# Kernel tuning notes

Measured on AMD Instinct MI355X. Metric: run time of the kernel, lower is better.

Reference implementation:

```python
import jax, jax.numpy as jnp
import numpy as np

ROUTE_SCALE = 2.5
TOP_K = 2
N_EXPERTS = 16


def setup_inputs() -> dict:
    key = jax.random.key(0)
    ks = jax.random.split(key, 8)
    B, T, D, I, E = 2, 1024, 768, 384, N_EXPERTS
    s = 0.02
    return {
        "x": jax.random.normal(ks[0], (B, T, D), dtype=jnp.float32),
        "gate_w": jax.random.normal(ks[1], (E, D), dtype=jnp.float32) * s,
        "sg_w": jax.random.normal(ks[2], (I, D), dtype=jnp.float32) * s,
        "su_w": jax.random.normal(ks[3], (I, D), dtype=jnp.float32) * s,
        "sd_w": jax.random.normal(ks[4], (D, I), dtype=jnp.float32) * s,
        "rg_w": jax.random.normal(ks[5], (E, I, D), dtype=jnp.float32) * s,
        "ru_w": jax.random.normal(ks[6], (E, I, D), dtype=jnp.float32) * s,
        "rd_w": jax.random.normal(ks[7], (E, D, I), dtype=jnp.float32) * s,
    }


def _moe_forward(x, gate_w, sg_w, su_w, sd_w, rg_w, ru_w, rd_w):
    B, T, D = x.shape
    flat = x.reshape(-1, D)  # (N, D), N = B*T

    # ---- shared expert (SwiGLU FFN) ----
    g = flat @ sg_w.T
    u = flat @ su_w.T
    shared_out = (jax.nn.silu(g) * u) @ sd_w.T  # (N, D)

    # ---- gate: softmax(fp32) -> top-k -> renormalize ----
    logits = (flat @ gate_w.T) * ROUTE_SCALE  # (N, E)
    scores = jax.nn.softmax(logits.astype(jnp.float32), axis=-1)
    topk_w, topk_i = jax.lax.top_k(scores, TOP_K)  # (N, K)
    topk_w = topk_w / jnp.sum(topk_w, axis=-1, keepdims=True)
    topk_w = topk_w.astype(x.dtype)

    # aux load-balancing loss
    one_hot = jax.nn.one_hot(topk_i, N_EXPERTS, dtype=jnp.float32)  # (N, K, E)
    mask = one_hot.sum(axis=1)  # (N, E)
    f = mask.mean(axis=0)
    p = scores.mean(axis=0)
    aux_loss = jnp.sum(f * p) * N_EXPERTS

    # combine weights per (token, expert): sum_k w_k * [idx_k == e]
    combine = jnp.einsum("nk,nke->ne", topk_w, one_hot.astype(x.dtype))  # (N, E)

    # ---- routed experts as batched (grouped) SwiGLU GEMMs ----
    rg = jnp.einsum("nd,eid->nei", flat, rg_w)  # (N, E, I)
    ru = jnp.einsum("nd,eid->nei", flat, ru_w)
    rh = jax.nn.silu(rg) * ru  # (N, E, I)
    eo = jnp.einsum("nei,edi->ned", rh, rd_w)  # (N, E, D)
    routed_out = jnp.einsum("ned,ne->nd", eo, combine)  # (N, D)

    out = (shared_out + routed_out).reshape(B, T, D)
    return out, aux_loss


def reference(x, gate_w, sg_w, su_w, sd_w, rg_w, ru_w, rd_w):
    return _moe_forward(x, gate_w, sg_w, su_w, sd_w, rg_w, ru_w, rd_w)
```

## Files before the change

### kernel.cpp

```cpp
#include <hip/hip_runtime.h>
#include <math.h>

#define NTOK 2048
#define DDIM 768
#define IDIM 384
#define NEXP 16
#define XS_LD 776
#define HS_LD 392
#define NRT_MAX 144
#define NSHT 64
#define NWORK ((NSHT + NRT_MAX) * 6)
#define CHUNK (NWORK / 8)

typedef __attribute__((ext_vector_type(8))) short short8;
typedef __attribute__((ext_vector_type(4))) float f32x4;

__device__ __forceinline__ unsigned short f2bf(float f) {
    unsigned int u = __float_as_uint(f);
    unsigned int r = (u + 0x7fffu + ((u >> 16) & 1u)) >> 16;
    return (unsigned short)r;
}

#define WS_XB   1048576u
#define WS_W1F  4194304u
#define WS_WDF  24248320u
#define WS_H    34275328u

__global__ __launch_bounds__(256) void zero_init_kernel(
    float4* __restrict__ out4, int n4,
    int* counts, int* cursor, int* offs, float* p_sum) {
    int i = blockIdx.x * 256 + threadIdx.x;
    if (i < n4) out4[i] = make_float4(0.f, 0.f, 0.f, 0.f);
    if (blockIdx.x == 0) {
        int t = threadIdx.x;
        if (t < 16) { counts[t] = 0; cursor[t] = 0; p_sum[t] = 0.f; }
        if (t < 17) offs[t] = 0;
    }
}

__global__ __launch_bounds__(256) void conv_all_kernel(
    const float* __restrict__ x,
    const float* __restrict__ rgw, const float* __restrict__ ruw,
    const float* __restrict__ sgw, const float* __restrict__ suw,
    const float* __restrict__ rdw, const float* __restrict__ sdw,
    unsigned short* __restrict__ xb, unsigned short* __restrict__ w1f,
    unsigned short* __restrict__ wdf) {
    int b = blockIdx.x, tid = threadIdx.x;
    const float* s;
    unsigned short* dst;
    if (b < 768) {
        int i = b * 256 + tid;
        s = x + (size_t)i * 8;
        dst = xb + (size_t)i * 8;
    } else if (b < 768 + 288 * 17) {
        int bb = b - 768;
        int E = bb / 288, bx = bb % 288;
        const float* gsrc = (E == 16) ? sgw : rgw + (size_t)E * (IDIM * DDIM);
        const float* usrc = (E == 16) ? suw : ruw + (size_t)E * (IDIM * DDIM);
        int i = bx * 256 + tid;
        int lane = i & 63;
        int fi = i >> 6;
        int ks = fi % 24, rg = fi / 24;
        int b16 = rg >> 1, gu = rg & 1;
        s = (gu ? usrc : gsrc)
          + (size_t)(b16 * 16 + (lane & 15)) * DDIM + ks * 32 + (lane >> 4) * 8;
        dst = w1f + (size_t)E * (DDIM * DDIM) + (size_t)i * 8;
    } else {
        int bb = b - (768 + 288 * 17);
        int E = bb / 144, bx = bb % 144;
        const float* src = (E == 16) ? sdw : rdw + (size_t)E * (DDIM * IDIM);
        int i = bx * 256 + tid;
        int lane = i & 63;
        int fi = i >> 6;
        int ks = fi % 12, cg = fi / 12;
        s = src + (size_t)(cg * 16 + (lane & 15)) * IDIM + ks * 32 + (lane >> 4) * 8;
        dst = wdf + (size_t)E * (DDIM * IDIM) + (size_t)i * 8;
    }
    float4 v0 = *(const float4*)s, v1 = *(const float4*)(s + 4);
    short8 o;
    o[0]=f2bf(v0.x); o[1]=f2bf(v0.y); o[2]=f2bf(v0.z); o[3]=f2bf(v0.w);
    o[4]=f2bf(v1.x); o[5]=f2bf(v1.y); o[6]=f2bf(v1.z); o[7]=f2bf(v1.w);
    *(short8*)dst = o;
}

__global__ __launch_bounds__(256) void gate_kernel(
    const float* __restrict__ x, const float* __restrict__ gate_w,
    int* __restrict__ topk_i, float* __restrict__ topk_w,
    int* __restrict__ counts, float* __restrict__ p_sum) {
    __shared__ float p_blk[16];
    __shared__ int   c_blk[16];
    int tid = threadIdx.x;
    if (tid < 16) { p_blk[tid] = 0.f; c_blk[tid] = 0; }
    __syncthreads();

    int wave = tid >> 6, lane = tid & 63;
    int n = blockIdx.x * 4 + wave;
    int e = lane >> 2, q = lane & 3;
    const float4* xr = (const float4*)(x + (size_t)n * DDIM);
    const float4* wr = (const float4*)(gate_w + (size_t)e * DDIM);
    float s = 0.f;
    #pragma unroll 4
    for (int k = q * 48; k < q * 48 + 48; ++k) {
        float4 a = xr[k], b = wr[k];
        s += a.x * b.x + a.y * b.y + a.z * b.z + a.w * b.w;
    }
    s += __shfl_xor(s, 1);
    s += __shfl_xor(s, 2);
    float logit = s * 2.5f;

    float l[16];
    #pragma unroll
    for (int j = 0; j < 16; ++j) l[j] = __shfl(logit, j * 4);

    float m = l[0];
    #pragma unroll
    for (int j = 1; j < 16; ++j) m = fmaxf(m, l[j]);
    float sum = 0.f, sc[16];
    #pragma unroll
    for (int j = 0; j < 16; ++j) { sc[j] = __expf(l[j] - m); sum += sc[j]; }
    float inv = 1.f / sum;
    #pragma unroll
    for (int j = 0; j < 16; ++j) sc[j] *= inv;

    float b0 = -1.f; int i0 = 0;
    #pragma unroll
    for (int j = 0; j < 16; ++j) if (sc[j] > b0) { b0 = sc[j]; i0 = j; }
    float b1 = -1.f; int i1 = 0;
    #pragma unroll
    for (int j = 0; j < 16; ++j) if (j != i0 && sc[j] > b1) { b1 = sc[j]; i1 = j; }
    float rs = 1.f / (b0 + b1);

    if (lane == 0) {
        topk_i[n * 2] = i0; topk_i[n * 2 + 1] = i1;
        topk_w[n * 2] = b0 * rs; topk_w[n * 2 + 1] = b1 * rs;
        atomicAdd(&c_blk[i0], 1); atomicAdd(&c_blk[i1], 1);
        #pragma unroll
        for (int j = 0; j < 16; ++j) atomicAdd(&p_blk[j], sc[j]);
    }
    __syncthreads();
    if (tid < 16) {
        atomicAdd(&p_sum[tid], p_blk[tid]);
        atomicAdd(&counts[tid], c_blk[tid]);
    }
}

__global__ __launch_bounds__(256) void route_kernel(
    const int* __restrict__ counts, const float* __restrict__ p_sum,
    const int* __restrict__ topk_i, const float* __restrict__ topk_w,
    int* __restrict__ offs, int* __restrict__ perm_t, float* __restrict__ perm_w,
    int* __restrict__ tile_e, int* __restrict__ tile_m, int* __restrict__ n_rt,
    float* __restrict__ out_aux) {
    __shared__ int s_off[17];
    __shared__ int s_cur[16];
    int tid = threadIdx.x;
    if (tid < 16) s_cur[tid] = 0;
    if (tid == 0) {
        int acc = 0, n = 0;
        float a = 0.f;
        for (int e = 0; e < 16; ++e) {
            int c = counts[e];
            s_off[e] = acc; offs[e] = acc;
            a += (float)c * p_sum[e];
            for (int t = 0; t < c; t += 32) { tile_e[n] = e; tile_m[n] = acc + t; ++n; }
            acc += c;
        }
        s_off[16] = acc; offs[16] = acc;
        *n_rt = n;
        out_aux[0] = a * 16.f / ((float)NTOK * (float)NTOK);
    }
    __syncthreads();
    for (int n0 = tid; n0 < NTOK; n0 += 256) {
        #pragma unroll
        for (int k = 0; k < 2; ++k) {
            int e = topk_i[n0 * 2 + k];
            int pos = atomicAdd(&s_cur[e], 1);
            int s = s_off[e] + pos;
            perm_t[s] = n0;
            perm_w[s] = topk_w[n0 * 2 + k];
        }
    }
}

__device__ __forceinline__ void swz_decode(int lid, int& bx, int& y) {
    int wid = (lid & 7) * CHUNK + (lid >> 3);
    bx = wid / 6;
    y = wid - bx * 6;
}

__global__ __launch_bounds__(256, 3) void p1_kernel(
    const unsigned short* __restrict__ xb, const unsigned short* __restrict__ w1f,
    const int* __restrict__ perm_t,
    const int* __restrict__ offs, const int* __restrict__ counts,
    const int* __restrict__ tile_e, const int* __restrict__ tile_m,
    const int* __restrict__ n_rt,
    unsigned short* __restrict__ h) {
    __shared__ unsigned short xs[32 * XS_LD];
    __shared__ int s_tok[32];
    __shared__ int s_hrow[32];

    int tid = threadIdx.x;
    int bx, y;
    swz_decode(blockIdx.x, bx, y);
    int e;
    if (bx < NSHT) {
        e = 16;
        if (tid < 32) { int t = bx * 32 + tid; s_tok[tid] = t; s_hrow[tid] = 4096 + t; }
    } else {
        int r = bx - NSHT;
        if (r >= *n_rt) return;
        e = tile_e[r];
        int m0 = tile_m[r];
        int end = offs[e] + counts[e];
        if (tid < 32) {
            int slot = m0 + tid;
            bool v = slot < end;
            s_tok[tid]  = v ? perm_t[slot] : 0;
            s_hrow[tid] = v ? slot : 6144 + tid;
        }
    }
    __syncthreads();

    for (int c = tid; c < 32 * 96; c += 256) {
        int row = c / 96, off = (c - row * 96) * 8;
        *(short8*)(xs + row * XS_LD + off) =
            *(const short8*)(xb + (size_t)s_tok[row] * DDIM + off);
    }
    __syncthreads();

    int lane = tid & 63, wave = tid >> 6;
    int lr = lane & 15, kg = (lane >> 4) * 8, jrow = (lane >> 4) * 4;

    const unsigned short* pg = w1f + ((((size_t)e * 48 + (y * 8 + wave * 2    )) * 24) * 64 + lane) * 8;
    const unsigned short* pu = w1f + ((((size_t)e * 48 + (y * 8 + wave * 2 + 1)) * 24) * 64 + lane) * 8;

    f32x4 accg0 = (f32x4)0.f, accg1 = (f32x4)0.f, accu0 = (f32x4)0.f, accu1 = (f32x4)0.f;
    for (int ks = 0; ks < 24; ++ks) {
        short8 a0 = *(const short8*)(xs + lr * XS_LD + ks * 32 + kg);
        short8 a1 = *(const short8*)(xs + (16 + lr) * XS_LD + ks * 32 + kg);
        short8 bg = *(const short8*)(pg + (size_t)ks * 512);
        short8 bu = *(const short8*)(pu + (size_t)ks * 512);
        accg0 = __builtin_amdgcn_mfma_f32_16x16x32_bf16(a0, bg, accg0, 0, 0, 0);
        accg1 = __builtin_amdgcn_mfma_f32_16x16x32_bf16(a1, bg, accg1, 0, 0, 0);
        accu0 = __builtin_amdgcn_mfma_f32_16x16x32_bf16(a0, bu, accu0, 0, 0, 0);
        accu1 = __builtin_amdgcn_mfma_f32_16x16x32_bf16(a1, bu, accu1, 0, 0, 0);
    }

    int colg = y * 64 + wave * 16 + lr;
    #pragma unroll
    for (int m = 0; m < 2; ++m) {
        #pragma unroll
        for (int j = 0; j < 4; ++j) {
            int tl = m * 16 + jrow + j;
            float g = m ? accg1[j] : accg0[j];
            float u = m ? accu1[j] : accu0[j];
            float hv = g / (1.f + __expf(-g)) * u;
            h[(size_t)s_hrow[tl] * IDIM + colg] = f2bf(hv);
        }
    }
}

__global__ __launch_bounds__(256, 4) void p2_kernel(
    const unsigned short* __restrict__ h, const unsigned short* __restrict__ wdf,
    const int* __restrict__ perm_t, const float* __restrict__ perm_w,
    const int* __restrict__ offs, const int* __restrict__ counts,
    const int* __restrict__ tile_e, const int* __restrict__ tile_m,
    const int* __restrict__ n_rt,
    float* __restrict__ out) {
    __shared__ unsigned short hs[32 * HS_LD];
    __shared__ int   s_tok[32];
    __shared__ float s_w[32];
    __shared__ int   s_arow[32];

    int tid = threadIdx.x;
    int bx, y;
    swz_decode(blockIdx.x, bx, y);
    int e;
    if (bx < NSHT) {
        e = 16;
        if (tid < 32) {
            int t = bx * 32 + tid;
            s_tok[tid] = t; s_w[tid] = 1.f; s_arow[tid] = 4096 + t;
        }
    } else {
        int r = bx - NSHT;
        if (r >= *n_rt) return;
        e = tile_e[r];
        int m0 = tile_m[r];
        int end = offs[e] + counts[e];
        if (tid < 32) {
            int slot = m0 + tid;
            bool v = slot < end;
            s_tok[tid]  = v ? perm_t[slot] : 0;
            s_w[tid]    = v ? perm_w[slot] : 0.f;
            s_arow[tid] = v ? slot : offs[e];
        }
    }
    __syncthreads();

    for (int c = tid; c < 32 * 48; c += 256) {
        int row = c / 48, off = (c - row * 48) * 8;
        *(short8*)(hs + row * HS_LD + off) =
            *(const short8*)(h + (size_t)s_arow[row] * IDIM + off);
    }
    __syncthreads();

    int lane = tid & 63, wave = tid >> 6;
    int lr = lane & 15, kg = (lane >> 4) * 8, jrow = (lane >> 4) * 4;

    const unsigned short* p0 = wdf + ((((size_t)e * 48 + (y * 8 + wave * 2    )) * 12) * 64 + lane) * 8;
    const unsigned short* p1 = wdf + ((((size_t)e * 48 + (y * 8 + wave * 2 + 1)) * 12) * 64 + lane) * 8;

    f32x4 acc00 = (f32x4)0.f, acc01 = (f32x4)0.f, acc10 = (f32x4)0.f, acc11 = (f32x4)0.f;
    for (int ks = 0; ks < 12; ++ks) {
        short8 a0 = *(const short8*)(hs + lr * HS_LD + ks * 32 + kg);
        short8 a1 = *(const short8*)(hs + (16 + lr) * HS_LD + ks * 32 + kg);
        short8 b0 = *(const short8*)(p0 + (size_t)ks * 512);
        short8 b1 = *(const short8*)(p1 + (size_t)ks * 512);
        acc00 = __builtin_amdgcn_mfma_f32_16x16x32_bf16(a0, b0, acc00, 0, 0, 0);
        acc01 = __builtin_amdgcn_mfma_f32_16x16x32_bf16(a1, b0, acc01, 0, 0, 0);
        acc10 = __builtin_amdgcn_mfma_f32_16x16x32_bf16(a0, b1, acc10, 0, 0, 0);
        acc11 = __builtin_amdgcn_mfma_f32_16x16x32_bf16(a1, b1, acc11, 0, 0, 0);
    }

    int col0 = y * 128 + wave * 32 + lr;
    #pragma unroll
    for (int m = 0; m < 2; ++m) {
        #pragma unroll
        for (int j = 0; j < 4; ++j) {
            int tl = m * 16 + jrow + j;
            float w = s_w[tl];
            if (w == 0.f) continue;
            float* orow = out + (size_t)s_tok[tl] * DDIM;
            float v0 = m ? acc01[j] : acc00[j];
            float v1 = m ? acc11[j] : acc10[j];
            atomicAdd(orow + col0,      w * v0);
            atomicAdd(orow + col0 + 16, w * v1);
        }
    }
}

extern "C" void kernel_launch(void* const* d_in, const int* in_sizes, int n_in,
                              void* d_out, int out_size, void* d_ws, size_t ws_size,
                              hipStream_t stream) {
    const float* x      = (const float*)d_in[0];
    const float* gate_w = (const float*)d_in[1];
    const float* sg_w   = (const float*)d_in[2];
    const float* su_w   = (const float*)d_in[3];
    const float* sd_w   = (const float*)d_in[4];
    const float* rg_w   = (const float*)d_in[5];
    const float* ru_w   = (const float*)d_in[6];
    const float* rd_w   = (const float*)d_in[7];
    float* out = (float*)d_out;

    char* ws = (char*)d_ws;
    int*   counts = (int*)(ws + 0);
    int*   cursor = (int*)(ws + 64);
    int*   offs   = (int*)(ws + 128);
    float* p_sum  = (float*)(ws + 256);
    int*   n_rt   = (int*)(ws + 320);
    int*   topk_i = (int*)(ws + 512);
    float* topk_w = (float*)(ws + 16896);
    int*   perm_t = (int*)(ws + 33280);
    float* perm_w = (float*)(ws + 49664);
    int*   tile_e = (int*)(ws + 66048);
    int*   tile_m = (int*)(ws + 66688);
    unsigned short* xb  = (unsigned short*)(ws + WS_XB);
    unsigned short* w1f = (unsigned short*)(ws + WS_W1F);
    unsigned short* wdf = (unsigned short*)(ws + WS_WDF);
    unsigned short* hbuf= (unsigned short*)(ws + WS_H);

    zero_init_kernel<<<1536, 256, 0, stream>>>(
        (float4*)out, NTOK * DDIM / 4, counts, cursor, offs, p_sum);

    conv_all_kernel<<<768 + 288 * 17 + 144 * 17, 256, 0, stream>>>(
        x, rg_w, ru_w, sg_w, su_w, rd_w, sd_w, xb, w1f, wdf);

    gate_kernel<<<NTOK / 4, 256, 0, stream>>>(x, gate_w, topk_i, topk_w, counts, p_sum);

    route_kernel<<<1, 256, 0, stream>>>(counts, p_sum, topk_i, topk_w,
                                        offs, perm_t, perm_w, tile_e, tile_m, n_rt,
                                        out + (size_t)NTOK * DDIM);

    p1_kernel<<<NWORK, 256, 0, stream>>>(
        xb, w1f, perm_t, offs, counts, tile_e, tile_m, n_rt, hbuf);
    p2_kernel<<<NWORK, 256, 0, stream>>>(
        hbuf, wdf, perm_t, perm_w, offs, counts, tile_e, tile_m, n_rt, out);
}
```

Measured before the change: 111.0 us.

## Fuse zero/convert/gate into one prep kernel and drop the routing kernel

Merges output zeroing, bf16 weight conversion and gating into a single launch. Routing now scatters tokens directly into fixed-capacity per-expert slots through global atomics, so the serial single-block route kernel goes away. The GEMM kernels find their tile by scanning the expert counts, and the aux loss moves into an extra p1 block. This cuts launches and a serial bottleneck, at the cost of slot order depending on atomic timing and a larger sparse h buffer.

```diff
diff --git a/kernel.cpp b/kernel.cpp
--- a/kernel.cpp
+++ b/kernel.cpp
@@ -11,6 +11,12 @@
 #define NSHT 64
 #define NWORK ((NSHT + NRT_MAX) * 6)
 #define CHUNK (NWORK / 8)
+#define ECAP 2048
+#define HSHARED (NEXP * ECAP)
+
+#define ZBLK 1536
+#define CBLK (768 + 288 * 17 + 144 * 17)
+#define GBLK (NTOK / 4)
 
 typedef __attribute__((ext_vector_type(8))) short short8;
 typedef __attribute__((ext_vector_type(4))) float f32x4;
@@ -26,83 +32,84 @@
 #define WS_WDF  24248320u
 #define WS_H    34275328u
 
-__global__ __launch_bounds__(256) void zero_init_kernel(
-    float4* __restrict__ out4, int n4,
-    int* counts, int* cursor, int* offs, float* p_sum) {
-    int i = blockIdx.x * 256 + threadIdx.x;
-    if (i < n4) out4[i] = make_float4(0.f, 0.f, 0.f, 0.f);
-    if (blockIdx.x == 0) {
-        int t = threadIdx.x;
-        if (t < 16) { counts[t] = 0; cursor[t] = 0; p_sum[t] = 0.f; }
-        if (t < 17) offs[t] = 0;
-    }
-}
-
-__global__ __launch_bounds__(256) void conv_all_kernel(
-    const float* __restrict__ x,
+__global__ __launch_bounds__(64) void init_kernel(int* cursor, float* p_sum) {
+    int t = threadIdx.x;
+    if (t < 16) { cursor[t] = 0; p_sum[t] = 0.f; }
+}
+
+__global__ __launch_bounds__(256) void prep_kernel(
+    const float* __restrict__ x, const float* __restrict__ gate_w,
     const float* __restrict__ rgw, const float* __restrict__ ruw,
     const float* __restrict__ sgw, const float* __restrict__ suw,
     const float* __restrict__ rdw, const float* __restrict__ sdw,
+    float4* __restrict__ out4,
     unsigned short* __restrict__ xb, unsigned short* __restrict__ w1f,
-    unsigned short* __restrict__ wdf) {
+    unsigned short* __restrict__ wdf,
+    int* __restrict__ cursor, float* __restrict__ p_sum,
+    int* __restrict__ perm_t, float* __restrict__ perm_w) {
     int b = blockIdx.x, tid = threadIdx.x;
-    const float* s;
-    unsigned short* dst;
-    if (b < 768) {
+
+    if (b < ZBLK) {
         int i = b * 256 + tid;
-        s = x + (size_t)i * 8;
-        dst = xb + (size_t)i * 8;
-    } else if (b < 768 + 288 * 17) {
-        int bb = b - 768;
-        int E = bb / 288, bx = bb % 288;
-        const float* gsrc = (E == 16) ? sgw : rgw + (size_t)E * (IDIM * DDIM);
-        const float* usrc = (E == 16) ? suw : ruw + (size_t)E * (IDIM * DDIM);
-        int i = bx * 256 + tid;
-        int lane = i & 63;
-        int fi = i >> 6;
-        int ks = fi % 24, rg = fi / 24;
-        int b16 = rg >> 1, gu = rg & 1;
-        s = (gu ? usrc : gsrc)
-          + (size_t)(b16 * 16 + (lane & 15)) * DDIM + ks * 32 + (lane >> 4) * 8;
-        dst = w1f + (size_t)E * (DDIM * DDIM) + (size_t)i * 8;
-    } else {
-        int bb = b - (768 + 288 * 17);
-        int E = bb / 144, bx = bb % 144;
-        const float* src = (E == 16) ? sdw : rdw + (size_t)E * (DDIM * IDIM);
-        int i = bx * 256 + tid;
-        int lane = i & 63;
-        int fi = i >> 6;
-        int ks = fi % 12, cg = fi / 12;
-        s = src + (size_t)(cg * 16 + (lane & 15)) * IDIM + ks * 32 + (lane >> 4) * 8;
-        dst = wdf + (size_t)E * (DDIM * IDIM) + (size_t)i * 8;
-    }
-    float4 v0 = *(const float4*)s, v1 = *(const float4*)(s + 4);
-    short8 o;
-    o[0]=f2bf(v0.x); o[1]=f2bf(v0.y); o[2]=f2bf(v0.z); o[3]=f2bf(v0.w);
-    o[4]=f2bf(v1.x); o[5]=f2bf(v1.y); o[6]=f2bf(v1.z); o[7]=f2bf(v1.w);
-    *(short8*)dst = o;
-}
-
-__global__ __launch_bounds__(256) void gate_kernel(
-    const float* __restrict__ x, const float* __restrict__ gate_w,
-    int* __restrict__ topk_i, float* __restrict__ topk_w,
-    int* __restrict__ counts, float* __restrict__ p_sum) {
+        if (i < NTOK * DDIM / 4) out4[i] = make_float4(0.f, 0.f, 0.f, 0.f);
+        return;
+    }
+    b -= ZBLK;
+
+    if (b < CBLK) {
+        const float* s;
+        unsigned short* dst;
+        if (b < 768) {
+            int i = b * 256 + tid;
+            s = x + (size_t)i * 8;
+            dst = xb + (size_t)i * 8;
+        } else if (b < 768 + 288 * 17) {
+            int bb = b - 768;
+            int E = bb / 288, bx = bb % 288;
+            const float* gsrc = (E == 16) ? sgw : rgw + (size_t)E * (IDIM * DDIM);
+            const float* usrc = (E == 16) ? suw : ruw + (size_t)E * (IDIM * DDIM);
+            int i = bx * 256 + tid;
+            int lane = i & 63;
+            int fi = i >> 6;
+            int ks = fi % 24, rg = fi / 24;
+            int b16 = rg >> 1, gu = rg & 1;
+            s = (gu ? usrc : gsrc)
+              + (size_t)(b16 * 16 + (lane & 15)) * DDIM + ks * 32 + (lane >> 4) * 8;
+            dst = w1f + (size_t)E * (DDIM * DDIM) + (size_t)i * 8;
+        } else {
+            int bb = b - (768 + 288 * 17);
+            int E = bb / 144, bx = bb % 144;
+            const float* src = (E == 16) ? sdw : rdw + (size_t)E * (DDIM * IDIM);
+            int i = bx * 256 + tid;
+            int lane = i & 63;
+            int fi = i >> 6;
+            int ks = fi % 12, cg = fi / 12;
+            s = src + (size_t)(cg * 16 + (lane & 15)) * IDIM + ks * 32 + (lane >> 4) * 8;
+            dst = wdf + (size_t)E * (DDIM * IDIM) + (size_t)i * 8;
+        }
+        float4 v0 = *(const float4*)s, v1 = *(const float4*)(s + 4);
+        short8 o;
+        o[0]=f2bf(v0.x); o[1]=f2bf(v0.y); o[2]=f2bf(v0.z); o[3]=f2bf(v0.w);
+        o[4]=f2bf(v1.x); o[5]=f2bf(v1.y); o[6]=f2bf(v1.z); o[7]=f2bf(v1.w);
+        *(short8*)dst = o;
+        return;
+    }
+    b -= CBLK;
+
     __shared__ float p_blk[16];
-    __shared__ int   c_blk[16];
-    int tid = threadIdx.x;
-    if (tid < 16) { p_blk[tid] = 0.f; c_blk[tid] = 0; }
+    if (tid < 16) p_blk[tid] = 0.f;
     __syncthreads();
 
     int wave = tid >> 6, lane = tid & 63;
-    int n = blockIdx.x * 4 + wave;
+    int n = b * 4 + wave;
     int e = lane >> 2, q = lane & 3;
     const float4* xr = (const float4*)(x + (size_t)n * DDIM);
     const float4* wr = (const float4*)(gate_w + (size_t)e * DDIM);
     float s = 0.f;
     #pragma unroll 4
     for (int k = q * 48; k < q * 48 + 48; ++k) {
-        float4 a = xr[k], b = wr[k];
-        s += a.x * b.x + a.y * b.y + a.z * b.z + a.w * b.w;
+        float4 a = xr[k], bb = wr[k];
+        s += a.x * bb.x + a.y * bb.y + a.z * bb.z + a.w * bb.w;
     }
     s += __shfl_xor(s, 1);
     s += __shfl_xor(s, 2);
@@ -131,54 +138,17 @@
     float rs = 1.f / (b0 + b1);
 
     if (lane == 0) {
-        topk_i[n * 2] = i0; topk_i[n * 2 + 1] = i1;
-        topk_w[n * 2] = b0 * rs; topk_w[n * 2 + 1] = b1 * rs;
-        atomicAdd(&c_blk[i0], 1); atomicAdd(&c_blk[i1], 1);
+        int p0 = atomicAdd(&cursor[i0], 1);
+        perm_t[i0 * ECAP + p0] = n;
+        perm_w[i0 * ECAP + p0] = b0 * rs;
+        int p1 = atomicAdd(&cursor[i1], 1);
+        perm_t[i1 * ECAP + p1] = n;
+        perm_w[i1 * ECAP + p1] = b1 * rs;
         #pragma unroll
         for (int j = 0; j < 16; ++j) atomicAdd(&p_blk[j], sc[j]);
     }
     __syncthreads();
-    if (tid < 16) {
-        atomicAdd(&p_sum[tid], p_blk[tid]);
-        atomicAdd(&counts[tid], c_blk[tid]);
-    }
-}
-
-__global__ __launch_bounds__(256) void route_kernel(
-    const int* __restrict__ counts, const float* __restrict__ p_sum,
-    const int* __restrict__ topk_i, const float* __restrict__ topk_w,
-    int* __restrict__ offs, int* __restrict__ perm_t, float* __restrict__ perm_w,
-    int* __restrict__ tile_e, int* __restrict__ tile_m, int* __restrict__ n_rt,
-    float* __restrict__ out_aux) {
-    __shared__ int s_off[17];
-    __shared__ int s_cur[16];
-    int tid = threadIdx.x;
-    if (tid < 16) s_cur[tid] = 0;
-    if (tid == 0) {
-        int acc = 0, n = 0;
-        float a = 0.f;
-        for (int e = 0; e < 16; ++e) {
-            int c = counts[e];
-            s_off[e] = acc; offs[e] = acc;
-            a += (float)c * p_sum[e];
-            for (int t = 0; t < c; t += 32) { tile_e[n] = e; tile_m[n] = acc + t; ++n; }
-            acc += c;
-        }
-        s_off[16] = acc; offs[16] = acc;
-        *n_rt = n;
-        out_aux[0] = a * 16.f / ((float)NTOK * (float)NTOK);
-    }
-    __syncthreads();
-    for (int n0 = tid; n0 < NTOK; n0 += 256) {
-        #pragma unroll
-        for (int k = 0; k < 2; ++k) {
-            int e = topk_i[n0 * 2 + k];
-            int pos = atomicAdd(&s_cur[e], 1);
-            int s = s_off[e] + pos;
-            perm_t[s] = n0;
-            perm_w[s] = topk_w[n0 * 2 + k];
-        }
-    }
+    if (tid < 16) atomicAdd(&p_sum[tid], p_blk[tid]);
 }
 
 __device__ __forceinline__ void swz_decode(int lid, int& bx, int& y) {
@@ -187,35 +157,50 @@
     y = wid - bx * 6;
 }
 
+__device__ __forceinline__ bool tile_decode(const int* __restrict__ counts,
+                                            int r, int& e, int& t, int& cnt) {
+    int acc = 0;
+    for (int ee = 0; ee < NEXP; ++ee) {
+        int c = counts[ee];
+        int tiles = (c + 31) >> 5;
+        if (r < acc + tiles) { e = ee; t = r - acc; cnt = c; return true; }
+        acc += tiles;
+    }
+    return false;
+}
+
 __global__ __launch_bounds__(256, 3) void p1_kernel(
     const unsigned short* __restrict__ xb, const unsigned short* __restrict__ w1f,
+    const int* __restrict__ counts, const float* __restrict__ p_sum,
     const int* __restrict__ perm_t,
-    const int* __restrict__ offs, const int* __restrict__ counts,
-    const int* __restrict__ tile_e, const int* __restrict__ tile_m,
-    const int* __restrict__ n_rt,
-    unsigned short* __restrict__ h) {
+    unsigned short* __restrict__ h, float* __restrict__ out_aux) {
+    if (blockIdx.x == NWORK) {
+        if (threadIdx.x == 0) {
+            float a = 0.f;
+            for (int ee = 0; ee < 16; ++ee) a += (float)counts[ee] * p_sum[ee];
+            out_aux[0] = a * 16.f / ((float)NTOK * (float)NTOK);
+        }
+        return;
+    }
+
     __shared__ unsigned short xs[32 * XS_LD];
     __shared__ int s_tok[32];
-    __shared__ int s_hrow[32];
 
     int tid = threadIdx.x;
     int bx, y;
     swz_decode(blockIdx.x, bx, y);
-    int e;
+    int e, hbase;
     if (bx < NSHT) {
         e = 16;
-        if (tid < 32) { int t = bx * 32 + tid; s_tok[tid] = t; s_hrow[tid] = 4096 + t; }
+        hbase = HSHARED + bx * 32;
+        if (tid < 32) s_tok[tid] = bx * 32 + tid;
     } else {
-        int r = bx - NSHT;
-        if (r >= *n_rt) return;
-        e = tile_e[r];
-        int m0 = tile_m[r];
-        int end = offs[e] + counts[e];
+        int t, cnt;
+        if (!tile_decode(counts, bx - NSHT, e, t, cnt)) return;
+        hbase = e * ECAP + t * 32;
         if (tid < 32) {
-            int slot = m0 + tid;
-            bool v = slot < end;
-            s_tok[tid]  = v ? perm_t[slot] : 0;
-            s_hrow[tid] = v ? slot : 6144 + tid;
+            int slot = t * 32 + tid;
+            s_tok[tid] = (slot < cnt) ? perm_t[e * ECAP + slot] : 0;
         }
     }
     __syncthreads();
@@ -254,45 +239,37 @@
             float g = m ? accg1[j] : accg0[j];
             float u = m ? accu1[j] : accu0[j];
             float hv = g / (1.f + __expf(-g)) * u;
-            h[(size_t)s_hrow[tl] * IDIM + colg] = f2bf(hv);
+            h[(size_t)(hbase + tl) * IDIM + colg] = f2bf(hv);
         }
     }
 }
 
 __global__ __launch_bounds__(256, 4) void p2_kernel(
     const unsigned short* __restrict__ h, const unsigned short* __restrict__ wdf,
+    const int* __restrict__ counts,
     const int* __restrict__ perm_t, const float* __restrict__ perm_w,
-    const int* __restrict__ offs, const int* __restrict__ counts,
-    const int* __restrict__ tile_e, const int* __restrict__ tile_m,
-    const int* __restrict__ n_rt,
     float* __restrict__ out) {
     __shared__ unsigned short hs[32 * HS_LD];
     __shared__ int   s_tok[32];
     __shared__ float s_w[32];
-    __shared__ int   s_arow[32];
 
     int tid = threadIdx.x;
     int bx, y;
     swz_decode(blockIdx.x, bx, y);
-    int e;
+    int e, hbase;
     if (bx < NSHT) {
         e = 16;
+        hbase = HSHARED + bx * 32;
+        if (tid < 32) { s_tok[tid] = bx * 32 + tid; s_w[tid] = 1.f; }
+    } else {
+        int t, cnt;
+        if (!tile_decode(counts, bx - NSHT, e, t, cnt)) return;
+        hbase = e * ECAP + t * 32;
         if (tid < 32) {
-            int t = bx * 32 + tid;
-            s_tok[tid] = t; s_w[tid] = 1.f; s_arow[tid] = 4096 + t;
-        }
-    } else {
-        int r = bx - NSHT;
-        if (r >= *n_rt) return;
-        e = tile_e[r];
-        int m0 = tile_m[r];
-        int end = offs[e] + counts[e];
-        if (tid < 32) {
-            int slot = m0 + tid;
-            bool v = slot < end;
-            s_tok[tid]  = v ? perm_t[slot] : 0;
-            s_w[tid]    = v ? perm_w[slot] : 0.f;
-            s_arow[tid] = v ? slot : offs[e];
+            int slot = t * 32 + tid;
+            bool v = slot < cnt;
+            s_tok[tid] = v ? perm_t[e * ECAP + slot] : 0;
+            s_w[tid]   = v ? perm_w[e * ECAP + slot] : 0.f;
         }
     }
     __syncthreads();
@@ -300,7 +277,7 @@
     for (int c = tid; c < 32 * 48; c += 256) {
         int row = c / 48, off = (c - row * 48) * 8;
         *(short8*)(hs + row * HS_LD + off) =
-            *(const short8*)(h + (size_t)s_arow[row] * IDIM + off);
+            *(const short8*)(h + (size_t)(hbase + row) * IDIM + off);
     }
     __syncthreads();
 
@@ -353,36 +330,24 @@
     float* out = (float*)d_out;
 
     char* ws = (char*)d_ws;
-    int*   counts = (int*)(ws + 0);
-    int*   cursor = (int*)(ws + 64);
-    int*   offs   = (int*)(ws + 128);
-    float* p_sum  = (float*)(ws + 256);
-    int*   n_rt   = (int*)(ws + 320);
-    int*   topk_i = (int*)(ws + 512);
-    float* topk_w = (float*)(ws + 16896);
-    int*   perm_t = (int*)(ws + 33280);
-    float* perm_w = (float*)(ws + 49664);
-    int*   tile_e = (int*)(ws + 66048);
-    int*   tile_m = (int*)(ws + 66688);
+    int*   cursor = (int*)(ws + 0);
+    float* p_sum  = (float*)(ws + 64);
+    int*   perm_t = (int*)(ws + 1024);
+    float* perm_w = (float*)(ws + 132096);
     unsigned short* xb  = (unsigned short*)(ws + WS_XB);
     unsigned short* w1f = (unsigned short*)(ws + WS_W1F);
     unsigned short* wdf = (unsigned short*)(ws + WS_WDF);
     unsigned short* hbuf= (unsigned short*)(ws + WS_H);
 
-    zero_init_kernel<<<1536, 256, 0, stream>>>(
-        (float4*)out, NTOK * DDIM / 4, counts, cursor, offs, p_sum);
-
-    conv_all_kernel<<<768 + 288 * 17 + 144 * 17, 256, 0, stream>>>(
-        x, rg_w, ru_w, sg_w, su_w, rd_w, sd_w, xb, w1f, wdf);
-
-    gate_kernel<<<NTOK / 4, 256, 0, stream>>>(x, gate_w, topk_i, topk_w, counts, p_sum);
-
-    route_kernel<<<1, 256, 0, stream>>>(counts, p_sum, topk_i, topk_w,
-                                        offs, perm_t, perm_w, tile_e, tile_m, n_rt,
-                                        out + (size_t)NTOK * DDIM);
-
-    p1_kernel<<<NWORK, 256, 0, stream>>>(
-        xb, w1f, perm_t, offs, counts, tile_e, tile_m, n_rt, hbuf);
+    init_kernel<<<1, 64, 0, stream>>>(cursor, p_sum);
+
+    prep_kernel<<<ZBLK + CBLK + GBLK, 256, 0, stream>>>(
+        x, gate_w, rg_w, ru_w, sg_w, su_w, rd_w, sd_w,
+        (float4*)out, xb, w1f, wdf, cursor, p_sum, perm_t, perm_w);
+
+    p1_kernel<<<NWORK + 1, 256, 0, stream>>>(
+        xb, w1f, cursor, p_sum, perm_t, hbuf, out + (size_t)NTOK * DDIM);
+
     p2_kernel<<<NWORK, 256, 0, stream>>>(
-        hbuf, wdf, perm_t, perm_w, offs, counts, tile_e, tile_m, n_rt, out);
-}
+        hbuf, wdf, cursor, perm_t, perm_w, out);
+}
```

Result: slower. 141.4 us (+27.4%).
